# Optimization experiments

Hardware: AMD Instinct MI355X
Metric: run time of the kernel (lower is better)

Reference implementation:

```python
import jax, jax.numpy as jnp
import numpy as np

B, H, SQ, SKV, D = 4, 16, 2048, 2048, 128
SCALE = float(np.sqrt(D))  # scale_factor passed to forward; q_k is divided by it


def setup_inputs() -> dict:
    key = jax.random.key(0)
    kq, kk, kv = jax.random.split(key, 3)
    q = jax.random.normal(kq, (B, H, SQ, D), dtype=jnp.float32)
    k = jax.random.normal(kk, (B, H, SKV, D), dtype=jnp.float32)
    v = jax.random.normal(kv, (B, H, SKV, D), dtype=jnp.float32)
    return {"q": q, "k": k, "v": v}


def reference(q, k, v):
    # q_k = q @ k^T, divided by scale_factor
    scores = jnp.einsum("bhqd,bhkd->bhqk", q, k) / SCALE  # [B,H,Sq,Skv]
    attn = jax.nn.softmax(scores, axis=-1)
    # dropout(p=0.1) is identity in eval/inference mode
    out = jnp.einsum("bhqk,bhkd->bhqd", attn, v)  # [B,H,Sq,D]
    return out
```

## Files before the change

### kernel.cpp

```cpp
#include <hip/hip_runtime.h>
#include <hip/hip_bf16.h>

#define B_ 4
#define H_ 16
#define SQ 2048
#define SKV 2048
#define D_ 128
#define BH (B_*H_)
#define BM 128
#define BN 64
#define NITER (SKV/BN)

typedef __attribute__((ext_vector_type(8))) short bf16x8;
typedef __attribute__((ext_vector_type(4))) float f32x4;
typedef __attribute__((ext_vector_type(16))) float f32x16;

__device__ inline unsigned short f2bf(float f) {
    union { float f; unsigned u; } x{f};
    unsigned r = x.u + 0x7fffu + ((x.u >> 16) & 1u);
    return (unsigned short)(r >> 16);
}

#if defined(__has_builtin) && __has_builtin(__builtin_amdgcn_cvt_pk_bf16_f32)
#define PKBF16(a,b) ({ auto _r = __builtin_amdgcn_cvt_pk_bf16_f32((a),(b)); \
                       unsigned _u; __builtin_memcpy(&_u, &_r, 4); _u; })
#else
#define PKBF16(a,b) ((unsigned)f2bf(a) | ((unsigned)f2bf(b) << 16))
#endif

__device__ inline void gl_lds16(const short* g, short* l) {
    __builtin_amdgcn_global_load_lds((const __attribute__((address_space(1))) unsigned*)g,
                                     (__attribute__((address_space(3))) unsigned*)l,
                                     16, 0, 0);
}

__device__ inline void pl32swap(unsigned &a, unsigned &b) {
#if defined(__has_builtin) && __has_builtin(__builtin_amdgcn_permlane32_swap)
    auto r = __builtin_amdgcn_permlane32_swap((int)a, (int)b, false, false);
    unsigned t[2]; __builtin_memcpy(t, &r, 8);
    a = t[0]; b = t[1];
#else
    int lane = threadIdx.x & 63;
    unsigned ap = __shfl(a, lane ^ 32);
    unsigned bp = __shfl(b, lane ^ 32);
    unsigned X = (lane < 32) ? a : bp;
    unsigned Y = (lane < 32) ? ap : b;
    a = X; b = Y;
#endif
}

__global__ __launch_bounds__(256) void prep(const float* __restrict__ kin,
                                            const float* __restrict__ vin,
                                            short* __restrict__ kbf,
                                            short* __restrict__ vtg) {
    int bx = blockIdx.x, tid = threadIdx.x;
    if (bx < 8192) {
        const float4* s = (const float4*)kin;
        uint2* d = (uint2*)kbf;
        int i = bx * 256 + tid;
        const int HALF = (BH * SKV * D_ / 4) / 2;
#pragma unroll
        for (int h = 0; h < 2; ++h) {
            int j = i + h * HALF;
            float4 a = s[j];
            d[j] = make_uint2(PKBF16(a.x, a.y), PKBF16(a.z, a.w));
        }
    } else {
        int bx2 = bx - 8192;
        int bh = bx2 >> 5;
        int t0 = (bx2 & 31) * 64;
        int w    = tid >> 6;
        int lane = tid & 63;
        int vg   = lane >> 3;
        int dc   = w * 32 + (lane & 7) * 4;
        const float* src = vin + ((size_t)bh * SKV + t0 + vg * 8) * D_ + dc;
        f32x4 vb[8];
#pragma unroll
        for (int t = 0; t < 8; ++t)
            vb[t] = *(const f32x4*)(src + (size_t)t * D_);
#pragma unroll
        for (int i = 0; i < 4; ++i) {
            const int d = dc + i;
            union { unsigned w4[4]; uint4 q; } o;
            o.w4[0] = PKBF16(vb[0][i], vb[1][i]);
            o.w4[1] = PKBF16(vb[2][i], vb[3][i]);
            o.w4[2] = PKBF16(vb[4][i], vb[5][i]);
            o.w4[3] = PKBF16(vb[6][i], vb[7][i]);
            *(uint4*)(vtg + ((size_t)bh * D_ + d) * SKV + t0 + vg * 8) = o.q;
        }
    }
}

__global__ __launch_bounds__(256, 2) void fa_kernel(const float* __restrict__ q,
                                                    const short* __restrict__ kbf,
                                                    const short* __restrict__ vtg,
                                                    float* __restrict__ out) {
    __shared__ short Ksh[2 * 64 * 128];
    __shared__ short Vsh[2 * 128 * 64];

    const int tid = threadIdx.x;
    const int wave = tid >> 6;
    const int lane = tid & 63;
    const int l32 = lane & 31;
    const int hi  = lane >> 5;

    const int bx = blockIdx.x;
    const int qt = bx & 15;
    const int bh = bx >> 4;
    const int qrow0 = qt * BM + wave * 32;

    const float cscale = 1.4426950408889634f * 0.08838834764831845f;

    bf16x8 qf[8];
    {
        const float* qp = q + ((size_t)bh * SQ + qrow0 + l32) * D_ + hi * 8;
#pragma unroll
        for (int dk = 0; dk < 8; ++dk) {
            float4 a = *(const float4*)(qp + dk * 16);
            float4 b = *(const float4*)(qp + dk * 16 + 4);
            union { unsigned u[4]; bf16x8 v; } f;
            f.u[0] = PKBF16(a.x * cscale, a.y * cscale);
            f.u[1] = PKBF16(a.z * cscale, a.w * cscale);
            f.u[2] = PKBF16(b.x * cscale, b.y * cscale);
            f.u[3] = PKBF16(b.z * cscale, b.w * cscale);
            qf[dk] = f.v;
        }
    }

    f32x16 oacc[4];
#pragma unroll
    for (int dt = 0; dt < 4; ++dt) oacc[dt] = (f32x16)0.f;
    float lsum = 0.f;

    const short* kbase = kbf + (size_t)bh * SKV * D_;
    const short* vbase = vtg + (size_t)bh * D_ * SKV;
    const int krow0 = wave * 4 + (lane >> 4);
    const int kc8 = (lane & 15) ^ krow0;
    const short* kg = kbase + krow0 * 128 + kc8 * 8;
    const int vd0 = wave * 8 + (lane >> 3);
    const int vc = (lane & 7) ^ (lane >> 3);
    const short* vg = vbase + (size_t)vd0 * SKV + vc * 8;

#define STAGE(b)                                                        \
    do {                                                                \
        short* klb = Ksh + (b) * 8192 + wave * 512;                     \
        short* vlb = Vsh + (b) * 8192 + wave * 512;                     \
        _Pragma("unroll")                                               \
        for (int s = 0; s < 4; ++s) {                                   \
            gl_lds16(kg + s * 2048, klb + s * 2048);                    \
            gl_lds16(vg + (size_t)s * 32 * SKV, vlb + s * 2048);        \
        }                                                               \
        kg += BN * D_;                                                  \
        vg += BN;                                                       \
    } while (0)

    STAGE(0);

    for (int it = 0; it < NITER; ++it) {
        __syncthreads();
        if (it + 1 < NITER) STAGE((it + 1) & 1);

        const short* Kc = Ksh + (it & 1) * 8192;
        const short* Vc = Vsh + (it & 1) * 8192;

#pragma unroll
        for (int kvt = 0; kvt < 2; ++kvt) {
            f32x16 sacc = (f32x16)0.f;
#pragma unroll
            for (int dk = 0; dk < 8; ++dk) {
                bf16x8 kf = *(const bf16x8*)&Kc[(kvt * 32 + l32) * 128 + (((dk * 2 + hi) ^ (lane & 15)) << 3)];
                sacc = __builtin_amdgcn_mfma_f32_32x32x16_bf16(kf, qf[dk], sacc, 0, 0, 0);
            }

            unsigned u[8];
            float ls = 0.f;
#pragma unroll
            for (int t = 0; t < 8; ++t) {
                float p0 = __builtin_amdgcn_exp2f(sacc[2 * t]);
                float p1 = __builtin_amdgcn_exp2f(sacc[2 * t + 1]);
                ls += p0 + p1;
                u[t] = PKBF16(p0, p1);
            }
            lsum += ls;

            pl32swap(u[0], u[2]);
            pl32swap(u[1], u[3]);
            pl32swap(u[4], u[6]);
            pl32swap(u[5], u[7]);
            union { unsigned w[4]; bf16x8 v; } pf0, pf1;
            pf0.w[0] = u[0]; pf0.w[1] = u[1]; pf0.w[2] = u[2]; pf0.w[3] = u[3];
            pf1.w[0] = u[4]; pf1.w[1] = u[5]; pf1.w[2] = u[6]; pf1.w[3] = u[7];

#pragma unroll
            for (int dt = 0; dt < 4; ++dt) {
                bf16x8 vf0 = *(const bf16x8*)&Vc[(dt * 32 + l32) * 64 + (((kvt * 4 + hi) ^ (lane & 7)) << 3)];
                oacc[dt] = __builtin_amdgcn_mfma_f32_32x32x16_bf16(vf0, pf0.v, oacc[dt], 0, 0, 0);
                bf16x8 vf1 = *(const bf16x8*)&Vc[(dt * 32 + l32) * 64 + (((kvt * 4 + 2 + hi) ^ (lane & 7)) << 3)];
                oacc[dt] = __builtin_amdgcn_mfma_f32_32x32x16_bf16(vf1, pf1.v, oacc[dt], 0, 0, 0);
            }
        }
    }
#undef STAGE

    lsum += __shfl_xor(lsum, 32);
    const float rl = 1.0f / lsum;
    float* op = out + ((size_t)bh * SQ + qrow0 + l32) * D_ + hi * 4;
#pragma unroll
    for (int dt = 0; dt < 4; ++dt)
#pragma unroll
        for (int g = 0; g < 4; ++g) {
            f32x4 v;
            v[0] = oacc[dt][4 * g + 0] * rl;
            v[1] = oacc[dt][4 * g + 1] * rl;
            v[2] = oacc[dt][4 * g + 2] * rl;
            v[3] = oacc[dt][4 * g + 3] * rl;
            *(f32x4*)(op + dt * 32 + g * 8) = v;
        }
}

extern "C" void kernel_launch(void* const* d_in, const int* in_sizes, int n_in,
                              void* d_out, int out_size, void* d_ws, size_t ws_size,
                              hipStream_t stream) {
    const float* q = (const float*)d_in[0];
    const float* k = (const float*)d_in[1];
    const float* v = (const float*)d_in[2];
    float* out = (float*)d_out;

    short* kbf = (short*)d_ws;
    short* vtg = kbf + (size_t)BH * SKV * D_;

    prep<<<8192 + 2048, 256, 0, stream>>>(k, v, kbf, vtg);
    fa_kernel<<<BH * (SQ / BM), 256, 0, stream>>>(q, kbf, vtg, out);
}
```

Measured before the change: 371.7 us.

## Fuse K fp32-to-bf16 conversion into attention kernel and remap blocks per XCD

Drops the separate K conversion pass from the prep kernel. The attention kernel now loads fp32 K straight into registers, converts it to bf16 and writes it into a single swizzled LDS buffer, with an extra barrier per iteration. This removes one full write and re-read of a bf16 copy of K through HBM, but every query tile now converts K again and the K prefetch goes through registers instead of async global-to-LDS loads. Block indices are also remapped so that all q-tiles of a given head land on the same XCD, improving L2 reuse of K and V.

```diff
diff --git a/kernel.cpp b/kernel.cpp
--- a/kernel.cpp
+++ b/kernel.cpp
@@ -49,53 +49,37 @@
 #endif
 }
 
-__global__ __launch_bounds__(256) void prep(const float* __restrict__ kin,
-                                            const float* __restrict__ vin,
-                                            short* __restrict__ kbf,
+__global__ __launch_bounds__(256) void prep(const float* __restrict__ vin,
                                             short* __restrict__ vtg) {
-    int bx = blockIdx.x, tid = threadIdx.x;
-    if (bx < 8192) {
-        const float4* s = (const float4*)kin;
-        uint2* d = (uint2*)kbf;
-        int i = bx * 256 + tid;
-        const int HALF = (BH * SKV * D_ / 4) / 2;
-#pragma unroll
-        for (int h = 0; h < 2; ++h) {
-            int j = i + h * HALF;
-            float4 a = s[j];
-            d[j] = make_uint2(PKBF16(a.x, a.y), PKBF16(a.z, a.w));
-        }
-    } else {
-        int bx2 = bx - 8192;
-        int bh = bx2 >> 5;
-        int t0 = (bx2 & 31) * 64;
-        int w    = tid >> 6;
-        int lane = tid & 63;
-        int vg   = lane >> 3;
-        int dc   = w * 32 + (lane & 7) * 4;
-        const float* src = vin + ((size_t)bh * SKV + t0 + vg * 8) * D_ + dc;
-        f32x4 vb[8];
-#pragma unroll
-        for (int t = 0; t < 8; ++t)
-            vb[t] = *(const f32x4*)(src + (size_t)t * D_);
-#pragma unroll
-        for (int i = 0; i < 4; ++i) {
-            const int d = dc + i;
-            union { unsigned w4[4]; uint4 q; } o;
-            o.w4[0] = PKBF16(vb[0][i], vb[1][i]);
-            o.w4[1] = PKBF16(vb[2][i], vb[3][i]);
-            o.w4[2] = PKBF16(vb[4][i], vb[5][i]);
-            o.w4[3] = PKBF16(vb[6][i], vb[7][i]);
-            *(uint4*)(vtg + ((size_t)bh * D_ + d) * SKV + t0 + vg * 8) = o.q;
-        }
+    int bx2 = blockIdx.x, tid = threadIdx.x;
+    int bh = bx2 >> 5;
+    int t0 = (bx2 & 31) * 64;
+    int w    = tid >> 6;
+    int lane = tid & 63;
+    int vg   = lane >> 3;
+    int dc   = w * 32 + (lane & 7) * 4;
+    const float* src = vin + ((size_t)bh * SKV + t0 + vg * 8) * D_ + dc;
+    f32x4 vb[8];
+#pragma unroll
+    for (int t = 0; t < 8; ++t)
+        vb[t] = *(const f32x4*)(src + (size_t)t * D_);
+#pragma unroll
+    for (int i = 0; i < 4; ++i) {
+        const int d = dc + i;
+        union { unsigned w4[4]; uint4 q; } o;
+        o.w4[0] = PKBF16(vb[0][i], vb[1][i]);
+        o.w4[1] = PKBF16(vb[2][i], vb[3][i]);
+        o.w4[2] = PKBF16(vb[4][i], vb[5][i]);
+        o.w4[3] = PKBF16(vb[6][i], vb[7][i]);
+        *(uint4*)(vtg + ((size_t)bh * D_ + d) * SKV + t0 + vg * 8) = o.q;
     }
 }
 
 __global__ __launch_bounds__(256, 2) void fa_kernel(const float* __restrict__ q,
-                                                    const short* __restrict__ kbf,
+                                                    const float* __restrict__ kin,
                                                     const short* __restrict__ vtg,
                                                     float* __restrict__ out) {
-    __shared__ short Ksh[2 * 64 * 128];
+    __shared__ short Ksh[64 * 128];
     __shared__ short Vsh[2 * 128 * 64];
 
     const int tid = threadIdx.x;
@@ -104,9 +88,11 @@
     const int l32 = lane & 31;
     const int hi  = lane >> 5;
 
-    const int bx = blockIdx.x;
-    const int qt = bx & 15;
-    const int bh = bx >> 4;
+    const int bxo = blockIdx.x;
+    const int xcd = bxo & 7;
+    const int slot = bxo >> 3;
+    const int bh = (xcd << 3) | (slot >> 4);
+    const int qt = slot & 15;
     const int qrow0 = qt * BM + wave * 32;
 
     const float cscale = 1.4426950408889634f * 0.08838834764831845f;
@@ -132,35 +118,58 @@
     for (int dt = 0; dt < 4; ++dt) oacc[dt] = (f32x16)0.f;
     float lsum = 0.f;
 
-    const short* kbase = kbf + (size_t)bh * SKV * D_;
+    const int kr  = wave * 16 + (lane >> 2);
+    const int kc  = lane & 3;
+    const float* kp = kin + ((size_t)bh * SKV + kr) * D_ + kc * 32;
+    short* const krow = Ksh + kr * 128;
+    const int kr15 = kr & 15;
+
     const short* vbase = vtg + (size_t)bh * D_ * SKV;
-    const int krow0 = wave * 4 + (lane >> 4);
-    const int kc8 = (lane & 15) ^ krow0;
-    const short* kg = kbase + krow0 * 128 + kc8 * 8;
     const int vd0 = wave * 8 + (lane >> 3);
     const int vc = (lane & 7) ^ (lane >> 3);
     const short* vg = vbase + (size_t)vd0 * SKV + vc * 8;
 
-#define STAGE(b)                                                        \
+#define KWRITE(kb)                                                      \
     do {                                                                \
-        short* klb = Ksh + (b) * 8192 + wave * 512;                     \
-        short* vlb = Vsh + (b) * 8192 + wave * 512;                     \
         _Pragma("unroll")                                               \
-        for (int s = 0; s < 4; ++s) {                                   \
-            gl_lds16(kg + s * 2048, klb + s * 2048);                    \
-            gl_lds16(vg + (size_t)s * 32 * SKV, vlb + s * 2048);        \
+        for (int j = 0; j < 4; ++j) {                                   \
+            const int cj = kc * 4 + j;                                  \
+            union { unsigned w[4]; bf16x8 v; } o;                       \
+            o.w[0] = PKBF16(kb[2*j][0], kb[2*j][1]);                    \
+            o.w[1] = PKBF16(kb[2*j][2], kb[2*j][3]);                    \
+            o.w[2] = PKBF16(kb[2*j+1][0], kb[2*j+1][1]);                \
+            o.w[3] = PKBF16(kb[2*j+1][2], kb[2*j+1][3]);                \
+            *(bf16x8*)(krow + ((cj ^ kr15) << 3)) = o.v;                \
         }                                                               \
-        kg += BN * D_;                                                  \
-        vg += BN;                                                       \
     } while (0)
 
-    STAGE(0);
+    f32x4 kb[8];
+#pragma unroll
+    for (int t = 0; t < 8; ++t) kb[t] = *(const f32x4*)(kp + 4 * t);
+    kp += BN * D_;
+    {
+        short* vlb = Vsh + wave * 512;
+#pragma unroll
+        for (int s = 0; s < 4; ++s)
+            gl_lds16(vg + (size_t)s * 32 * SKV, vlb + s * 2048);
+        vg += BN;
+    }
+    KWRITE(kb);
 
     for (int it = 0; it < NITER; ++it) {
         __syncthreads();
-        if (it + 1 < NITER) STAGE((it + 1) & 1);
-
-        const short* Kc = Ksh + (it & 1) * 8192;
+
+        if (it + 1 < NITER) {
+#pragma unroll
+            for (int t = 0; t < 8; ++t) kb[t] = *(const f32x4*)(kp + 4 * t);
+            kp += BN * D_;
+            short* vlb = Vsh + ((it + 1) & 1) * 8192 + wave * 512;
+#pragma unroll
+            for (int s = 0; s < 4; ++s)
+                gl_lds16(vg + (size_t)s * 32 * SKV, vlb + s * 2048);
+            vg += BN;
+        }
+
         const short* Vc = Vsh + (it & 1) * 8192;
 
 #pragma unroll
@@ -168,7 +177,7 @@
             f32x16 sacc = (f32x16)0.f;
 #pragma unroll
             for (int dk = 0; dk < 8; ++dk) {
-                bf16x8 kf = *(const bf16x8*)&Kc[(kvt * 32 + l32) * 128 + (((dk * 2 + hi) ^ (lane & 15)) << 3)];
+                bf16x8 kf = *(const bf16x8*)&Ksh[(kvt * 32 + l32) * 128 + (((dk * 2 + hi) ^ (lane & 15)) << 3)];
                 sacc = __builtin_amdgcn_mfma_f32_32x32x16_bf16(kf, qf[dk], sacc, 0, 0, 0);
             }
 
@@ -199,8 +208,11 @@
                 oacc[dt] = __builtin_amdgcn_mfma_f32_32x32x16_bf16(vf1, pf1.v, oacc[dt], 0, 0, 0);
             }
         }
-    }
-#undef STAGE
+
+        __syncthreads();
+        if (it + 1 < NITER) KWRITE(kb);
+    }
+#undef KWRITE
 
     lsum += __shfl_xor(lsum, 32);
     const float rl = 1.0f / lsum;
@@ -226,9 +238,8 @@
     const float* v = (const float*)d_in[2];
     float* out = (float*)d_out;
 
-    short* kbf = (short*)d_ws;
-    short* vtg = kbf + (size_t)BH * SKV * D_;
-
-    prep<<<8192 + 2048, 256, 0, stream>>>(k, v, kbf, vtg);
-    fa_kernel<<<BH * (SQ / BM), 256, 0, stream>>>(q, kbf, vtg, out);
-}
+    short* vtg = (short*)d_ws;
+
+    prep<<<2048, 256, 0, stream>>>(v, vtg);
+    fa_kernel<<<BH * (SQ / BM), 256, 0, stream>>>(q, k, vtg, out);
+}
```

Result: slower. 493.4 us (+32.7%).
